# Kernel tuning notes

Hardware: AMD Instinct MI355X
Metric: run time of the kernel (lower is better)

Reference implementation:

```python
import jax, jax.numpy as jnp
import numpy as np

EPS = 1e-10

def setup_inputs() -> dict:
    key = jax.random.key(0)
    k1, k2 = jax.random.split(key)
    support_set = jax.random.normal(k1, (8192, 1024), dtype=jnp.float32)
    input_image = jax.random.normal(k2, (2048, 1024), dtype=jnp.float32)
    return {"support_set": support_set, "input_image": input_image}

def reference(support_set, input_image):
    # support_set: [n, d], input_image: [b, d]
    # Faithful to original: input magnitude is a single scalar over the whole
    # [b, d] input matrix; support magnitude is a scalar per support vector.
    input_mag = jax.lax.rsqrt(jnp.maximum(jnp.sum(input_image * input_image), EPS))  # scalar
    support_mag = jax.lax.rsqrt(jnp.maximum(jnp.sum(support_set * support_set, axis=1), EPS))  # [n]
    dot = jnp.einsum('bd,nd->nb', input_image, support_set)  # [n, b]
    sims = dot * support_mag[:, None] * input_mag  # [n, b]
    return sims[:, :, None]  # [n, b, 1] == torch.stack(...)[n,b,1].squeeze(1) (no-op for b>1)
```

## Files before the change

kernel.cpp:

```cpp
#include <hip/hip_runtime.h>
#include <hip/hip_bf16.h>
#include <stdint.h>
#include <stddef.h>

#define M_DIM 8192
#define N_DIM 2048
#define K_DIM 1024

#define BM 256
#define BN 256
#define BK 64
#define NKT (K_DIM / BK)
#define NITER (NKT / 2)

typedef __attribute__((ext_vector_type(8))) short short8;
typedef __attribute__((ext_vector_type(8))) unsigned short ushort8v;
typedef __attribute__((ext_vector_type(4))) float float4v;

static __device__ __forceinline__ unsigned short f2bf(float x) {
  union { float f; unsigned u; } c; c.f = x;
  return (unsigned short)((c.u + 0x7FFFu + ((c.u >> 16) & 1u)) >> 16);
}

#define GLOAD_LDS16(g, l)                                           \
  __builtin_amdgcn_global_load_lds(                                 \
      (const __attribute__((address_space(1))) void*)(g),           \
      (__attribute__((address_space(3))) void*)(l), 16, 0, 0)

__global__ __launch_bounds__(256) void prep(
    const float* __restrict__ S, const float* __restrict__ I,
    unsigned short* __restrict__ Sb, unsigned short* __restrict__ Ib,
    float* __restrict__ smag, float* __restrict__ partials) {
  const int t = threadIdx.x;
  const int lane = t & 63;
  const int wave = t >> 6;
  const int blk = blockIdx.x;
  const bool isS = blk < 2048;
  const int row = (isS ? blk : blk - 2048) * 4 + wave;
  const float4* s4 = reinterpret_cast<const float4*>((isS ? S : I) + (size_t)row * K_DIM);
  ushort8v* d8 = reinterpret_cast<ushort8v*>((isS ? Sb : Ib) + (size_t)row * K_DIM);

  float4 v[4];
  v[0] = s4[2 * lane];
  v[1] = s4[2 * lane + 1];
  v[2] = s4[128 + 2 * lane];
  v[3] = s4[128 + 2 * lane + 1];

  float ss = 0.f;
  ushort8v o0, o1;
#pragma unroll
  for (int h = 0; h < 2; ++h) {
    const float4 a = v[2 * h], b = v[2 * h + 1];
    ushort8v o;
    o[0] = f2bf(a.x); o[1] = f2bf(a.y); o[2] = f2bf(a.z); o[3] = f2bf(a.w);
    o[4] = f2bf(b.x); o[5] = f2bf(b.y); o[6] = f2bf(b.z); o[7] = f2bf(b.w);
    ss += a.x * a.x + a.y * a.y + a.z * a.z + a.w * a.w;
    ss += b.x * b.x + b.y * b.y + b.z * b.z + b.w * b.w;
    if (h == 0) o0 = o; else o1 = o;
  }
  d8[lane] = o0;
  d8[64 + lane] = o1;

#pragma unroll
  for (int m = 32; m >= 1; m >>= 1) ss += __shfl_xor(ss, m, 64);
  if (lane == 0) {
    if (isS) smag[row] = rsqrtf(fmaxf(ss, 1e-10f));
    else     partials[row] = ss;
  }
}

__global__ __launch_bounds__(512, 2) void gemm_bt(
    const unsigned short* __restrict__ A,
    const unsigned short* __restrict__ B,
    const float* __restrict__ smag,
    const float* __restrict__ partials,
    float* __restrict__ C) {
  __shared__ __align__(16) unsigned short lA[32768];
  __shared__ __align__(16) unsigned short lB[32768];
  __shared__ float wsum[8];

  const int t = threadIdx.x;
  const int lane = t & 63;
  const int wave = t >> 6;
  const int wr = wave >> 2;
  const int wc = wave & 3;

  const int blk = blockIdx.x;
  const int xcd = blk & 7;
  const int slot = blk >> 3;
  const int bm = (xcd * 4 + (slot & 3)) * BM;
  const int bn = (slot >> 2) * BN;

  {
    float p = partials[t] + partials[t + 512] + partials[t + 1024] + partials[t + 1536];
#pragma unroll
    for (int m = 32; m >= 1; m >>= 1) p += __shfl_xor(p, m, 64);
    if (lane == 0) wsum[wave] = p;
  }
  asm volatile("s_waitcnt vmcnt(0)" ::: "memory");

  const int srow = t >> 3;
  const int skc = (t & 7) ^ (srow & 7);
  const unsigned short* gA[4];
  const unsigned short* gB[4];
  int aoff[4];
#pragma unroll
  for (int j = 0; j < 4; ++j) {
    gA[j] = A + (size_t)(bm + j * 64 + srow) * K_DIM + skc * 8;
    gB[j] = B + (size_t)(bn + j * 64 + srow) * K_DIM + skc * 8;
    aoff[j] = (j >> 1) * 8192 + (j & 1) * 4096 + wave * 512;
  }

#define STAGE_A(j, buf) do { GLOAD_LDS16(gA[j], &lA[(buf) * 16384 + aoff[j]]); gA[j] += BK; } while (0)
#define STAGE_B(j, buf) do { GLOAD_LDS16(gB[j], &lB[(buf) * 16384 + aoff[j]]); gB[j] += BK; } while (0)
#define SP1(buf) do { STAGE_B(0, buf); STAGE_B(1, buf); } while (0)
#define SP2(buf) do { STAGE_B(2, buf); STAGE_B(3, buf); } while (0)
#define SP3(buf) do { STAGE_A(0, buf); STAGE_A(2, buf); } while (0)
#define SP4(buf) do { STAGE_A(1, buf); STAGE_A(3, buf); } while (0)

  const int fr = lane & 15;
  const int q = lane >> 4;
  const int pc0 = (q ^ (fr & 7)) * 8;
  const int pc1 = ((4 + q) ^ (fr & 7)) * 8;
  const unsigned short* rA = lA + wr * 8192 + fr * 64;
  const unsigned short* rB = lB + (wc >> 1) * 8192 + ((wc & 1) * 64 + fr) * 64;

  short8 af0[2][2], af1[2][2];
  short8 bfA[4][2], bfB[4][2];
  float4v acc[8][4];
#pragma unroll
  for (int i = 0; i < 8; ++i)
#pragma unroll
    for (int j = 0; j < 4; ++j) acc[i][j] = (float4v)0.0f;

#define BARRIER() __builtin_amdgcn_s_barrier()
#define VMW(n) asm volatile("s_waitcnt vmcnt(" #n ")" ::: "memory")
#define PRIO1() __builtin_amdgcn_s_setprio(1)
#define PRIO0() __builtin_amdgcn_s_setprio(0)
#define SGB(n) do {                                                            \
    __builtin_amdgcn_sched_group_barrier(0x100, n, 0);                         \
    __builtin_amdgcn_sched_group_barrier(0x008, 16, 0);                        \
  } while (0)

#define LOADB_LO(bank, buf) do {                                               \
    _Pragma("unroll") for (int nj = 0; nj < 2; ++nj) {                         \
      bank[nj][0] = *reinterpret_cast<const short8*>(rB + (buf) * 16384 + nj * 1024 + pc0); \
      bank[nj][1] = *reinterpret_cast<const short8*>(rB + (buf) * 16384 + nj * 1024 + pc1); \
    } } while (0)

#define LOADB_HI(bank, buf) do {                                               \
    _Pragma("unroll") for (int nj = 2; nj < 4; ++nj) {                         \
      bank[nj][0] = *reinterpret_cast<const short8*>(rB + (buf) * 16384 + nj * 1024 + pc0); \
      bank[nj][1] = *reinterpret_cast<const short8*>(rB + (buf) * 16384 + nj * 1024 + pc1); \
    } } while (0)

#define LOADA(bank, buf, pi) do {                                              \
    _Pragma("unroll") for (int m2 = 0; m2 < 2; ++m2) {                         \
      bank[m2][0] = *reinterpret_cast<const short8*>(rA + (buf) * 16384 + ((pi) * 2 + m2) * 1024 + pc0); \
      bank[m2][1] = *reinterpret_cast<const short8*>(rA + (buf) * 16384 + ((pi) * 2 + m2) * 1024 + pc1); \
    } } while (0)

#define MFMA16(pi, abank, bbank) do {                                          \
    PRIO1();                                                                   \
    _Pragma("unroll") for (int m2 = 0; m2 < 2; ++m2)                           \
    _Pragma("unroll") for (int nj = 0; nj < 4; ++nj) {                         \
      acc[(pi) * 2 + m2][nj] = __builtin_amdgcn_mfma_f32_16x16x32_bf16(        \
          abank[m2][0], bbank[nj][0], acc[(pi) * 2 + m2][nj], 0, 0, 0);        \
      acc[(pi) * 2 + m2][nj] = __builtin_amdgcn_mfma_f32_16x16x32_bf16(        \
          abank[m2][1], bbank[nj][1], acc[(pi) * 2 + m2][nj], 0, 0, 0);        \
    } } while (0)

#define ITER_F() do {                                                          \
     SP4(1);           BARRIER(); SGB(8);                             \
              LOADA(af1, 0, 1); LOADB_HI(bfA, 0); MFMA16(0, af0, bfA);         \
     SP1(0); VMW(10);  BARRIER(); SGB(4);                             \
              LOADA(af0, 0, 2); MFMA16(1, af1, bfA);                           \
     SP2(0);           BARRIER(); SGB(4);                             \
              LOADA(af1, 0, 3); MFMA16(2, af0, bfA);                           \
     SP3(0); VMW(8);   BARRIER(); SGB(8);                             \
              LOADB_LO(bfB, 1); LOADA(af0, 1, 0); MFMA16(3, af1, bfA);         \
     SP4(0);           BARRIER(); SGB(8);                             \
              LOADA(af1, 1, 1); LOADB_HI(bfB, 1); MFMA16(0, af0, bfB);         \
     SP1(1); VMW(10);  BARRIER(); SGB(4);                             \
              LOADA(af0, 1, 2); MFMA16(1, af1, bfB);                           \
     SP2(1);           BARRIER(); SGB(4);                             \
              LOADA(af1, 1, 3); MFMA16(2, af0, bfB);                           \
     SP3(1); VMW(8);   BARRIER(); SGB(8);                             \
              LOADB_LO(bfA, 0); LOADA(af0, 0, 0); MFMA16(3, af1, bfB);         \
  } while (0)

#define ITER_T() do {                                                          \
     SP4(1);           BARRIER(); SGB(8);                             \
              LOADA(af1, 0, 1); LOADB_HI(bfA, 0); MFMA16(0, af0, bfA);         \
     VMW(8);           BARRIER(); SGB(4);                             \
              LOADA(af0, 0, 2); MFMA16(1, af1, bfA);                           \
                       BARRIER(); SGB(4);                             \
              LOADA(af1, 0, 3); MFMA16(2, af0, bfA);                           \
     VMW(2);           BARRIER(); SGB(8);                             \
              LOADB_LO(bfB, 1); LOADA(af0, 1, 0); MFMA16(3, af1, bfA);         \
                       BARRIER(); SGB(8);                             \
              LOADA(af1, 1, 1); LOADB_HI(bfB, 1); MFMA16(0, af0, bfB);         \
     VMW(0);           BARRIER(); SGB(4);                             \
              LOADA(af0, 1, 2); MFMA16(1, af1, bfB);                           \
                       BARRIER(); SGB(4);                             \
              LOADA(af1, 1, 3); MFMA16(2, af0, bfB);                           \
                       BARRIER();                                     \
              MFMA16(3, af1, bfB);                                             \
  } while (0)

  SP1(0); SP2(0); SP3(0); SP4(0);
  SP1(1); SP2(1); SP3(1);
  VMW(6);
  BARRIER();
  LOADB_LO(bfA, 0); LOADB_HI(bfA, 0); LOADA(af0, 0, 0);

#pragma unroll 1
  for (int it = 0; it < NITER - 1; ++it) ITER_F();
  ITER_T();

  const float imag = rsqrtf(fmaxf(wsum[0] + wsum[1] + wsum[2] + wsum[3] +
                                  wsum[4] + wsum[5] + wsum[6] + wsum[7], 1e-10f));
#pragma unroll
  for (int mi = 0; mi < 8; ++mi) {
    const int rbase = bm + wr * 128 + mi * 16 + q * 4;
#pragma unroll
    for (int r = 0; r < 4; ++r) {
      const int row = rbase + r;
      const float sc = smag[row] * imag;
      float* crow = C + (size_t)row * N_DIM + bn + wc * 64 + fr;
#pragma unroll
      for (int nj = 0; nj < 4; ++nj) crow[nj * 16] = acc[mi][nj][r] * sc;
    }
  }
}

extern "C" void kernel_launch(void* const* d_in, const int* in_sizes, int n_in,
                              void* d_out, int out_size, void* d_ws, size_t ws_size,
                              hipStream_t stream) {
  const float* S = (const float*)d_in[0];
  const float* I = (const float*)d_in[1];
  float* out = (float*)d_out;

  unsigned char* ws = (unsigned char*)d_ws;
  unsigned short* Sb = (unsigned short*)ws;
  unsigned short* Ib = (unsigned short*)(ws + (size_t)M_DIM * K_DIM * 2);
  float* smag = (float*)(ws + (size_t)M_DIM * K_DIM * 2 + (size_t)N_DIM * K_DIM * 2);
  float* partials = smag + M_DIM;

  hipLaunchKernelGGL(prep, dim3(2560), dim3(256), 0, stream,
                     S, I, Sb, Ib, smag, partials);
  hipLaunchKernelGGL(gemm_bt, dim3((M_DIM / BM) * (N_DIM / BN)), dim3(512), 0, stream,
                     Sb, Ib, smag, partials, out);
}
```

Before: 124.3 us.

## Halve block barriers per k-iteration by merging MFMA phases into pairs

Regroups the main-loop schedule so each barrier covers two MFMA phases instead of one, which cuts the block-wide barriers per k-tile pair from eight to four. The vmcnt waits and scheduling-group hints are adjusted to the new phase boundaries. Fewer barriers mean less wave stalling, but the LDS stage writes and reads are now separated by fewer syncs. That relies on the buffer reuse distances still being safe and could add VGPR pressure from the wider scheduling windows.

Result: no change. 125.5 us (+1.0%).

```diff
diff --git a/kernel.cpp b/kernel.cpp
--- a/kernel.cpp
+++ b/kernel.cpp
@@ -137,9 +137,11 @@
 #define VMW(n) asm volatile("s_waitcnt vmcnt(" #n ")" ::: "memory")
 #define PRIO1() __builtin_amdgcn_s_setprio(1)
 #define PRIO0() __builtin_amdgcn_s_setprio(0)
-#define SGB(n) do {                                                            \
-    __builtin_amdgcn_sched_group_barrier(0x100, n, 0);                         \
-    __builtin_amdgcn_sched_group_barrier(0x008, 16, 0);                        \
+#define SGB2(r1, m1, r2, m2) do {                                              \
+    __builtin_amdgcn_sched_group_barrier(0x100, r1, 0);                        \
+    __builtin_amdgcn_sched_group_barrier(0x008, m1, 0);                        \
+    __builtin_amdgcn_sched_group_barrier(0x100, r2, 0);                        \
+    __builtin_amdgcn_sched_group_barrier(0x008, m2, 0);                        \
   } while (0)
 
 #define LOADB_LO(bank, buf) do {                                               \
@@ -171,41 +173,43 @@
     } } while (0)
 
 #define ITER_F() do {                                                          \
-     SP4(1);           BARRIER(); SGB(8);                             \
-              LOADA(af1, 0, 1); LOADB_HI(bfA, 0); MFMA16(0, af0, bfA);         \
-     SP1(0); VMW(10);  BARRIER(); SGB(4);                             \
-              LOADA(af0, 0, 2); MFMA16(1, af1, bfA);                           \
-     SP2(0);           BARRIER(); SGB(4);                             \
-              LOADA(af1, 0, 3); MFMA16(2, af0, bfA);                           \
-     SP3(0); VMW(8);   BARRIER(); SGB(8);                             \
-              LOADB_LO(bfB, 1); LOADA(af0, 1, 0); MFMA16(3, af1, bfA);         \
-     SP4(0);           BARRIER(); SGB(8);                             \
-              LOADA(af1, 1, 1); LOADB_HI(bfB, 1); MFMA16(0, af0, bfB);         \
-     SP1(1); VMW(10);  BARRIER(); SGB(4);                             \
-              LOADA(af0, 1, 2); MFMA16(1, af1, bfB);                           \
-     SP2(1);           BARRIER(); SGB(4);                             \
-              LOADA(af1, 1, 3); MFMA16(2, af0, bfB);                           \
-     SP3(1); VMW(8);   BARRIER(); SGB(8);                             \
-              LOADB_LO(bfA, 0); LOADA(af0, 0, 0); MFMA16(3, af1, bfB);         \
+                                                             \
+    SP4(1); VMW(8);  BARRIER(); SGB2(8, 16, 4, 16);                            \
+    LOADA(af1, 0, 1); LOADB_HI(bfA, 0); MFMA16(0, af0, bfA);                   \
+    SP1(0); LOADA(af0, 0, 2); MFMA16(1, af1, bfA);                             \
+                                                             \
+    SP2(0); VMW(6);  BARRIER(); SGB2(4, 16, 8, 16);                            \
+    LOADA(af1, 0, 3); MFMA16(2, af0, bfA);                                     \
+    SP3(0); LOADB_LO(bfB, 1); LOADA(af0, 1, 0); MFMA16(3, af1, bfA);           \
+                                                             \
+    SP4(0); VMW(8);  BARRIER(); SGB2(8, 16, 4, 16);                            \
+    LOADA(af1, 1, 1); LOADB_HI(bfB, 1); MFMA16(0, af0, bfB);                   \
+    SP1(1); LOADA(af0, 1, 2); MFMA16(1, af1, bfB);                             \
+                                                             \
+    SP2(1); VMW(6);  BARRIER(); SGB2(4, 16, 8, 16);                            \
+    LOADA(af1, 1, 3); MFMA16(2, af0, bfB);                                     \
+    SP3(1); LOADB_LO(bfA, 0); LOADA(af0, 0, 0); MFMA16(3, af1, bfB);           \
   } while (0)
 
 #define ITER_T() do {                                                          \
-     SP4(1);           BARRIER(); SGB(8);                             \
-              LOADA(af1, 0, 1); LOADB_HI(bfA, 0); MFMA16(0, af0, bfA);         \
-     VMW(8);           BARRIER(); SGB(4);                             \
-              LOADA(af0, 0, 2); MFMA16(1, af1, bfA);                           \
-                       BARRIER(); SGB(4);                             \
-              LOADA(af1, 0, 3); MFMA16(2, af0, bfA);                           \
-     VMW(2);           BARRIER(); SGB(8);                             \
-              LOADB_LO(bfB, 1); LOADA(af0, 1, 0); MFMA16(3, af1, bfA);         \
-                       BARRIER(); SGB(8);                             \
-              LOADA(af1, 1, 1); LOADB_HI(bfB, 1); MFMA16(0, af0, bfB);         \
-     VMW(0);           BARRIER(); SGB(4);                             \
-              LOADA(af0, 1, 2); MFMA16(1, af1, bfB);                           \
-                       BARRIER(); SGB(4);                             \
-              LOADA(af1, 1, 3); MFMA16(2, af0, bfB);                           \
-                       BARRIER();                                     \
-              MFMA16(3, af1, bfB);                                             \
+                                                                       \
+    SP4(1); VMW(8);  BARRIER(); SGB2(8, 16, 4, 16);                            \
+    LOADA(af1, 0, 1); LOADB_HI(bfA, 0); MFMA16(0, af0, bfA);                   \
+    LOADA(af0, 0, 2); MFMA16(1, af1, bfA);                                     \
+                                                                       \
+    VMW(2);          BARRIER(); SGB2(4, 16, 8, 16);                            \
+    LOADA(af1, 0, 3); MFMA16(2, af0, bfA);                                     \
+    LOADB_LO(bfB, 1); LOADA(af0, 1, 0); MFMA16(3, af1, bfA);                   \
+                                                                       \
+    VMW(0);          BARRIER(); SGB2(8, 16, 4, 16);                            \
+    LOADA(af1, 1, 1); LOADB_HI(bfB, 1); MFMA16(0, af0, bfB);                   \
+    LOADA(af0, 1, 2); MFMA16(1, af1, bfB);                                     \
+                                                                       \
+                     BARRIER();                                                \
+    __builtin_amdgcn_sched_group_barrier(0x100, 4, 0);                         \
+    __builtin_amdgcn_sched_group_barrier(0x008, 32, 0);                        \
+    LOADA(af1, 1, 3); MFMA16(2, af0, bfB);                                     \
+    MFMA16(3, af1, bfB);                                                       \
   } while (0)
 
   SP1(0); SP2(0); SP3(0); SP4(0);
```

## Stagger LDS-read/MFMA order between even and odd waves; load B fragments at once

Applied to the files above, without the earlier changes.

Splits the main loop into two variants. Even waves issue LDS fragment reads before their MFMAs, and odd waves issue MFMAs first and then reads, so waves sharing a SIMD alternate between LDS and matrix-core use instead of contending at the same time. B fragments are now loaded in one 4-column batch in the phase that previously loaded only the low half, and the high-half load is dropped from the following phase. This raises register pressure at that point and doubles the loop code size, and the benefit depends on how the hardware actually interleaves waves.

Result: slower. 126.9 us (+2.0%).

```diff
diff --git a/kernel.cpp b/kernel.cpp
--- a/kernel.cpp
+++ b/kernel.cpp
@@ -137,19 +137,17 @@
 #define VMW(n) asm volatile("s_waitcnt vmcnt(" #n ")" ::: "memory")
 #define PRIO1() __builtin_amdgcn_s_setprio(1)
 #define PRIO0() __builtin_amdgcn_s_setprio(0)
-#define SGB(n) do {                                                            \
+#define SGB_RM(n) do {                                                         \
     __builtin_amdgcn_sched_group_barrier(0x100, n, 0);                         \
     __builtin_amdgcn_sched_group_barrier(0x008, 16, 0);                        \
   } while (0)
-
-#define LOADB_LO(bank, buf) do {                                               \
-    _Pragma("unroll") for (int nj = 0; nj < 2; ++nj) {                         \
-      bank[nj][0] = *reinterpret_cast<const short8*>(rB + (buf) * 16384 + nj * 1024 + pc0); \
-      bank[nj][1] = *reinterpret_cast<const short8*>(rB + (buf) * 16384 + nj * 1024 + pc1); \
-    } } while (0)
-
-#define LOADB_HI(bank, buf) do {                                               \
-    _Pragma("unroll") for (int nj = 2; nj < 4; ++nj) {                         \
+#define SGB_MR(n) do {                                                         \
+    __builtin_amdgcn_sched_group_barrier(0x008, 16, 0);                        \
+    __builtin_amdgcn_sched_group_barrier(0x100, n, 0);                         \
+  } while (0)
+
+#define LOADB(bank, buf) do {                                                  \
+    _Pragma("unroll") for (int nj = 0; nj < 4; ++nj) {                         \
       bank[nj][0] = *reinterpret_cast<const short8*>(rB + (buf) * 16384 + nj * 1024 + pc0); \
       bank[nj][1] = *reinterpret_cast<const short8*>(rB + (buf) * 16384 + nj * 1024 + pc1); \
     } } while (0)
@@ -170,40 +168,78 @@
           abank[m2][1], bbank[nj][1], acc[(pi) * 2 + m2][nj], 0, 0, 0);        \
     } } while (0)
 
-#define ITER_F() do {                                                          \
-     SP4(1);           BARRIER(); SGB(8);                             \
-              LOADA(af1, 0, 1); LOADB_HI(bfA, 0); MFMA16(0, af0, bfA);         \
-     SP1(0); VMW(10);  BARRIER(); SGB(4);                             \
+#define ITER_F_E() do {                                                        \
+     SP4(1);           BARRIER(); SGB_RM(4);                          \
+              LOADA(af1, 0, 1); MFMA16(0, af0, bfA);                           \
+     SP1(0); VMW(10);  BARRIER(); SGB_RM(4);                          \
               LOADA(af0, 0, 2); MFMA16(1, af1, bfA);                           \
-     SP2(0);           BARRIER(); SGB(4);                             \
+     SP2(0);           BARRIER(); SGB_RM(4);                          \
               LOADA(af1, 0, 3); MFMA16(2, af0, bfA);                           \
-     SP3(0); VMW(8);   BARRIER(); SGB(8);                             \
-              LOADB_LO(bfB, 1); LOADA(af0, 1, 0); MFMA16(3, af1, bfA);         \
-     SP4(0);           BARRIER(); SGB(8);                             \
-              LOADA(af1, 1, 1); LOADB_HI(bfB, 1); MFMA16(0, af0, bfB);         \
-     SP1(1); VMW(10);  BARRIER(); SGB(4);                             \
+     SP3(0); VMW(8);   BARRIER(); SGB_RM(12);                         \
+              LOADB(bfB, 1); LOADA(af0, 1, 0); MFMA16(3, af1, bfA);            \
+     SP4(0);           BARRIER(); SGB_RM(4);                          \
+              LOADA(af1, 1, 1); MFMA16(0, af0, bfB);                           \
+     SP1(1); VMW(10);  BARRIER(); SGB_RM(4);                          \
               LOADA(af0, 1, 2); MFMA16(1, af1, bfB);                           \
-     SP2(1);           BARRIER(); SGB(4);                             \
+     SP2(1);           BARRIER(); SGB_RM(4);                          \
               LOADA(af1, 1, 3); MFMA16(2, af0, bfB);                           \
-     SP3(1); VMW(8);   BARRIER(); SGB(8);                             \
-              LOADB_LO(bfA, 0); LOADA(af0, 0, 0); MFMA16(3, af1, bfB);         \
-  } while (0)
-
-#define ITER_T() do {                                                          \
-     SP4(1);           BARRIER(); SGB(8);                             \
-              LOADA(af1, 0, 1); LOADB_HI(bfA, 0); MFMA16(0, af0, bfA);         \
-     VMW(8);           BARRIER(); SGB(4);                             \
+     SP3(1); VMW(8);   BARRIER(); SGB_RM(12);                         \
+              LOADB(bfA, 0); LOADA(af0, 0, 0); MFMA16(3, af1, bfB);            \
+  } while (0)
+
+#define ITER_T_E() do {                                                        \
+     SP4(1);           BARRIER(); SGB_RM(4);                          \
+              LOADA(af1, 0, 1); MFMA16(0, af0, bfA);                           \
+     VMW(8);           BARRIER(); SGB_RM(4);                          \
               LOADA(af0, 0, 2); MFMA16(1, af1, bfA);                           \
-                       BARRIER(); SGB(4);                             \
+                       BARRIER(); SGB_RM(4);                          \
               LOADA(af1, 0, 3); MFMA16(2, af0, bfA);                           \
-     VMW(2);           BARRIER(); SGB(8);                             \
-              LOADB_LO(bfB, 1); LOADA(af0, 1, 0); MFMA16(3, af1, bfA);         \
-                       BARRIER(); SGB(8);                             \
-              LOADA(af1, 1, 1); LOADB_HI(bfB, 1); MFMA16(0, af0, bfB);         \
-     VMW(0);           BARRIER(); SGB(4);                             \
+     VMW(2);           BARRIER(); SGB_RM(12);                         \
+              LOADB(bfB, 1); LOADA(af0, 1, 0); MFMA16(3, af1, bfA);            \
+                       BARRIER(); SGB_RM(4);                          \
+              LOADA(af1, 1, 1); MFMA16(0, af0, bfB);                           \
+     VMW(0);           BARRIER(); SGB_RM(4);                          \
               LOADA(af0, 1, 2); MFMA16(1, af1, bfB);                           \
-                       BARRIER(); SGB(4);                             \
+                       BARRIER(); SGB_RM(4);                          \
               LOADA(af1, 1, 3); MFMA16(2, af0, bfB);                           \
+                       BARRIER();                                     \
+              MFMA16(3, af1, bfB);                                             \
+  } while (0)
+
+#define ITER_F_O() do {                                                        \
+     SP4(1);           BARRIER(); SGB_MR(4);                          \
+              MFMA16(0, af0, bfA); LOADA(af1, 0, 1);                           \
+     SP1(0); VMW(10);  BARRIER(); SGB_MR(4);                          \
+              MFMA16(1, af1, bfA); LOADA(af0, 0, 2);                           \
+     SP2(0);           BARRIER(); SGB_MR(4);                          \
+              MFMA16(2, af0, bfA); LOADA(af1, 0, 3);                           \
+     SP3(0); VMW(8);   BARRIER(); SGB_MR(12);                         \
+              MFMA16(3, af1, bfA); LOADB(bfB, 1); LOADA(af0, 1, 0);            \
+     SP4(0);           BARRIER(); SGB_MR(4);                          \
+              MFMA16(0, af0, bfB); LOADA(af1, 1, 1);                           \
+     SP1(1); VMW(10);  BARRIER(); SGB_MR(4);                          \
+              MFMA16(1, af1, bfB); LOADA(af0, 1, 2);                           \
+     SP2(1);           BARRIER(); SGB_MR(4);                          \
+              MFMA16(2, af0, bfB); LOADA(af1, 1, 3);                           \
+     SP3(1); VMW(8);   BARRIER(); SGB_MR(12);                         \
+              MFMA16(3, af1, bfB); LOADB(bfA, 0); LOADA(af0, 0, 0);            \
+  } while (0)
+
+#define ITER_T_O() do {                                                        \
+     SP4(1);           BARRIER(); SGB_MR(4);                          \
+              MFMA16(0, af0, bfA); LOADA(af1, 0, 1);                           \
+     VMW(8);           BARRIER(); SGB_MR(4);                          \
+              MFMA16(1, af1, bfA); LOADA(af0, 0, 2);                           \
+                       BARRIER(); SGB_MR(4);                          \
+              MFMA16(2, af0, bfA); LOADA(af1, 0, 3);                           \
+     VMW(2);           BARRIER(); SGB_MR(12);                         \
+              MFMA16(3, af1, bfA); LOADB(bfB, 1); LOADA(af0, 1, 0);            \
+                       BARRIER(); SGB_MR(4);                          \
+              MFMA16(0, af0, bfB); LOADA(af1, 1, 1);                           \
+     VMW(0);           BARRIER(); SGB_MR(4);                          \
+              MFMA16(1, af1, bfB); LOADA(af0, 1, 2);                           \
+                       BARRIER(); SGB_MR(4);                          \
+              MFMA16(2, af0, bfB); LOADA(af1, 1, 3);                           \
                        BARRIER();                                     \
               MFMA16(3, af1, bfB);                                             \
   } while (0)
@@ -212,11 +248,17 @@
   SP1(1); SP2(1); SP3(1);
   VMW(6);
   BARRIER();
-  LOADB_LO(bfA, 0); LOADB_HI(bfA, 0); LOADA(af0, 0, 0);
-
+  LOADB(bfA, 0); LOADA(af0, 0, 0);
+
+  if ((wave & 1) == 0) {
 #pragma unroll 1
-  for (int it = 0; it < NITER - 1; ++it) ITER_F();
-  ITER_T();
+    for (int it = 0; it < NITER - 1; ++it) ITER_F_E();
+    ITER_T_E();
+  } else {
+#pragma unroll 1
+    for (int it = 0; it < NITER - 1; ++it) ITER_F_O();
+    ITER_T_O();
+  }
 
   const float imag = rsqrtf(fmaxf(wsum[0] + wsum[1] + wsum[2] + wsum[3] +
                                   wsum[4] + wsum[5] + wsum[6] + wsum[7], 1e-10f));
```
